# Optimization experiments

Measured on AMD Instinct MI355X. Metric: run time of the kernel, lower is better.

The kernel has to match this reference:

```python
import jax, jax.numpy as jnp
import numpy as np

NEG_BIG = -9e15
ALPHA = 0.2  # leakyrelu negative slope

N, F_IN, F_OUT = 8192, 512, 64


def setup_inputs() -> dict:
    key = jax.random.key(0)
    k1, k2, k3, k4 = jax.random.split(key, 4)
    input = jax.random.normal(k1, (N, F_IN), dtype=jnp.float32)
    adj = jax.random.randint(k2, (N, N), 0, 2, dtype=jnp.int32)
    W = jax.random.normal(k3, (F_IN, F_OUT), dtype=jnp.float32) * 0.05
    a = jax.random.normal(k4, (2 * F_OUT, 1), dtype=jnp.float32) * 0.1
    return {"input": input, "adj": adj, "W": W, "a": a}


def reference(input, adj, W, a):
    # h: [N, F_out]
    h = input @ W
    # The original builds a_input[i,j] = concat(h_i, h_j) and dots with a.
    # Decompose: e_ij = leakyrelu(h_i @ a_src + h_j @ a_dst) -- identical math,
    # avoids the N*N*2F intermediate.
    a_src = a[:F_OUT, 0]  # [F_out]
    a_dst = a[F_OUT:, 0]  # [F_out]
    s_src = h @ a_src     # [N]
    s_dst = h @ a_dst     # [N]
    e = jax.nn.leaky_relu(s_src[:, None] + s_dst[None, :], negative_slope=ALPHA)  # [N, N]
    masked = jnp.where(adj > 0, e, jnp.float32(NEG_BIG))
    attention = jax.nn.softmax(masked, axis=1)  # dropout omitted (eval mode)
    h_prime = attention @ h  # [N, F_out]
    return jax.nn.elu(h_prime)  # concat=True
```

## Files before the change

kernel.cpp:

```cpp
#include <hip/hip_runtime.h>
#include <hip/hip_bf16.h>

namespace {
constexpr int kN    = 8192;
constexpr int kFin  = 512;
constexpr int kFout = 64;
constexpr float kAlpha = 0.2f;
constexpr int kJSplit = 4;
constexpr int kJLen   = kN / kJSplit;
constexpr int kChunks = kJLen / 128;

using bf16x8 = __attribute__((ext_vector_type(8))) short;
using f32x4  = __attribute__((ext_vector_type(4))) float;

__device__ __forceinline__ unsigned short f2bf(float x) {
  return __builtin_bit_cast(unsigned short, __float2bfloat16(x));
}
__device__ __forceinline__ float lrelu(float x) {
  return fmaxf(x, kAlpha * x);
}
__device__ __forceinline__ unsigned int fkey(float x) {
  unsigned int b = __float_as_uint(x);
  return (b & 0x80000000u) ? ~b : (b | 0x80000000u);
}
__device__ __forceinline__ float fdec(unsigned int k) {
  return (k & 0x80000000u) ? __uint_as_float(k ^ 0x80000000u) : __uint_as_float(~k);
}
}

__global__ __launch_bounds__(256) void k_wt(const float* __restrict__ W,
                                            float* __restrict__ WT,
                                            unsigned int* __restrict__ Smax_u) {
  const int gid = blockIdx.x * 256 + threadIdx.x;
  if (gid == 0) *Smax_u = 0u;
  const int k = gid >> 6, f = gid & 63;
  WT[(size_t)f * kFin + k] = W[gid];
}

__global__ __launch_bounds__(256) void k_linear(
    const float* __restrict__ X, const float* __restrict__ WT, const float* __restrict__ A,
    unsigned short* __restrict__ hTf, float* __restrict__ s_src, float* __restrict__ s_dst,
    unsigned int* __restrict__ Smax_u)
{
  const int t = threadIdx.x;
  const int wv = t >> 6, f = t & 63;
  const int i0 = blockIdx.x * 16;

  __shared__ float Xlds[16 * kFin];
  __shared__ unsigned short h_sm[16][64];
  __shared__ float red[4];

  {
    const float4* Xg = (const float4*)(X + (size_t)i0 * kFin);
    float4* Xl = (float4*)Xlds;
    float4 v0 = Xg[t +   0], v1 = Xg[t + 256], v2 = Xg[t +  512], v3 = Xg[t +  768];
    float4 v4 = Xg[t +1024], v5 = Xg[t +1280], v6 = Xg[t + 1536], v7 = Xg[t + 1792];
    Xl[t +    0] = v0; Xl[t +  256] = v1; Xl[t +  512] = v2; Xl[t +  768] = v3;
    Xl[t + 1024] = v4; Xl[t + 1280] = v5; Xl[t + 1536] = v6; Xl[t + 1792] = v7;
  }
  __syncthreads();

  const int r0l = wv * 4;
  const float* w0 = WT + (size_t)f * kFin;
  float acc0 = 0.f, acc1 = 0.f, acc2 = 0.f, acc3 = 0.f;
  float4 wb0 = *(const float4*)(w0 + 0);
  float4 wb1 = *(const float4*)(w0 + 4);
  const float* xr = Xlds + r0l * kFin;
  for (int k = 0; k < kFin; k += 4) {
    const float4 wc = (k & 4) ? wb1 : wb0;
    if (k + 8 < kFin) {
      const float4 wn = *(const float4*)(w0 + k + 8);
      if (k & 4) wb1 = wn; else wb0 = wn;
    }
    const float4 xa = *(const float4*)(xr + k);
    const float4 xb = *(const float4*)(xr + kFin + k);
    const float4 xc = *(const float4*)(xr + 2 * kFin + k);
    const float4 xd = *(const float4*)(xr + 3 * kFin + k);
#pragma unroll
    for (int j = 0; j < 4; ++j) {
      const float wk = ((const float*)&wc)[j];
      acc0 = fmaf(((const float*)&xa)[j], wk, acc0);
      acc1 = fmaf(((const float*)&xb)[j], wk, acc1);
      acc2 = fmaf(((const float*)&xc)[j], wk, acc2);
      acc3 = fmaf(((const float*)&xd)[j], wk, acc3);
    }
  }

  const float asrc = A[f], adst = A[kFout + f];
  float accs[4] = {acc0, acc1, acc2, acc3};
  float dmax = -3.4e38f;
#pragma unroll
  for (int r = 0; r < 4; ++r) {
    float vs = accs[r] * asrc;
    float vd = accs[r] * adst;
#pragma unroll
    for (int off = 32; off > 0; off >>= 1) {
      vs += __shfl_xor(vs, off, 64);
      vd += __shfl_xor(vd, off, 64);
    }
    if (f == 0) {
      s_src[i0 + r0l + r] = vs;
      s_dst[i0 + r0l + r] = vd;
      dmax = fmaxf(dmax, vd);
    }
    h_sm[r0l + r][f] = f2bf(accs[r]);
  }
  if (f == 0) red[wv] = dmax;
  __syncthreads();
  if (t == 0) {
    float m = fmaxf(fmaxf(red[0], red[1]), fmaxf(red[2], red[3]));
    atomicMax(Smax_u, fkey(m));
  }

  if (t < 128) {
    const int jblk = i0 >> 5, half = (i0 >> 4) & 1;
    const int w = t >> 5, li = t & 31;
    const int lane = half * 32 + li;
    const int ql = li >> 4, fcol = w * 16 + (li & 15);
    bf16x8 v;
#pragma unroll
    for (int e = 0; e < 8; ++e) v[e] = (short)h_sm[ql * 8 + e][fcol];
    *(bf16x8*)(hTf + (size_t)jblk * 2048 + w * 512 + (size_t)lane * 8) = v;
  }
}

__global__ __launch_bounds__(256) void k_attn(
    const int* __restrict__ adj, const unsigned short* __restrict__ hTf,
    const float* __restrict__ s_src, const float* __restrict__ s_dst,
    const unsigned int* __restrict__ Smax_u, float* __restrict__ accp,
    float* __restrict__ lp)
{
  const int t = threadIdx.x;
  const int wv = t >> 6, lane = t & 63;
  const int b = blockIdx.x;
  const int i0 = (b >> 2) * 16;
  const int jbase = (b & 3) * kJLen;
  const int pr = t >> 4, jb = t & 15;

  __shared__ unsigned short Plds[2][16][136];

  const float S = fdec(*Smax_u);
  const float ssrc = s_src[i0 + pr];
  const float mr = lrelu(ssrc + S);

  float l_acc = 0.f;
  f32x4 acc = {0.f, 0.f, 0.f, 0.f};

  const int4*   aptr = (const int4*)(adj + (size_t)(i0 + pr) * kN + jbase + jb * 8);
  const float4* dptr = (const float4*)(s_dst + jbase + jb * 8);
  const unsigned short* hbase = hTf + (size_t)(jbase >> 5) * 2048 + wv * 512 + (size_t)lane * 8;

  const int mrow = lane & 15, quad = lane >> 4;

  int4   A0a = aptr[0],  A1a = aptr[1];
  float4 D0a = dptr[0],  D1a = dptr[1];
  int4   A0b = aptr[32], A1b = aptr[33];
  float4 D0b = dptr[32], D1b = dptr[33];

  auto phase = [&](int c, int sbuf, int4& A0, int4& A1, float4& D0, float4& D1)
      __attribute__((always_inline)) {
    float pv[8];
    {
      const int* aa = (const int*)&A0;
      const float* dd = (const float*)&D0;
#pragma unroll
      for (int j = 0; j < 4; ++j) {
        const float e = lrelu(ssrc + dd[j]);
        pv[j] = aa[j] > 0 ? __expf(e - mr) : 0.f;
      }
      aa = (const int*)&A1; dd = (const float*)&D1;
#pragma unroll
      for (int j = 0; j < 4; ++j) {
        const float e = lrelu(ssrc + dd[j]);
        pv[4 + j] = aa[j] > 0 ? __expf(e - mr) : 0.f;
      }
    }
    bf16x8 ps;
#pragma unroll
    for (int j = 0; j < 8; ++j) {
      l_acc += pv[j];
      ps[j] = (short)f2bf(pv[j]);
    }
    *(bf16x8*)&Plds[sbuf][pr][jb * 8] = ps;

    const uint4 hv0 = *(const uint4*)(hbase + (size_t)(c * 4 + 0) * 2048);
    const uint4 hv1 = *(const uint4*)(hbase + (size_t)(c * 4 + 1) * 2048);
    const uint4 hv2 = *(const uint4*)(hbase + (size_t)(c * 4 + 2) * 2048);
    const uint4 hv3 = *(const uint4*)(hbase + (size_t)(c * 4 + 3) * 2048);

    if (c + 2 < kChunks) {
      A0 = aptr[(c + 2) * 32]; A1 = aptr[(c + 2) * 32 + 1];
      D0 = dptr[(c + 2) * 32]; D1 = dptr[(c + 2) * 32 + 1];
    }
    __syncthreads();

    acc = __builtin_amdgcn_mfma_f32_16x16x32_bf16(
        *(const bf16x8*)&Plds[sbuf][mrow][0 * 32 + quad * 8], __builtin_bit_cast(bf16x8, hv0), acc, 0, 0, 0);
    acc = __builtin_amdgcn_mfma_f32_16x16x32_bf16(
        *(const bf16x8*)&Plds[sbuf][mrow][1 * 32 + quad * 8], __builtin_bit_cast(bf16x8, hv1), acc, 0, 0, 0);
    acc = __builtin_amdgcn_mfma_f32_16x16x32_bf16(
        *(const bf16x8*)&Plds[sbuf][mrow][2 * 32 + quad * 8], __builtin_bit_cast(bf16x8, hv2), acc, 0, 0, 0);
    acc = __builtin_amdgcn_mfma_f32_16x16x32_bf16(
        *(const bf16x8*)&Plds[sbuf][mrow][3 * 32 + quad * 8], __builtin_bit_cast(bf16x8, hv3), acc, 0, 0, 0);
  };

  for (int c = 0; c < kChunks; c += 2) {
    phase(c,     0, A0a, A1a, D0a, D1a);
    phase(c + 1, 1, A0b, A1b, D0b, D1b);
  }

  float lv = l_acc;
  lv += __shfl_xor(lv, 8, 64);
  lv += __shfl_xor(lv, 4, 64);
  lv += __shfl_xor(lv, 2, 64);
  lv += __shfl_xor(lv, 1, 64);
  if (jb == 0) lp[(size_t)b * 16 + pr] = lv;

  float* ab = accp + (size_t)b * 16 * 64;
#pragma unroll
  for (int reg = 0; reg < 4; ++reg) {
    ab[(quad * 4 + reg) * 64 + wv * 16 + mrow] = acc[reg];
  }
}

__global__ __launch_bounds__(256) void k_comb(const float* __restrict__ accp,
                                              const float* __restrict__ lp,
                                              float* __restrict__ out)
{
  const int gid = blockIdx.x * 256 + threadIdx.x;
  const int i = gid >> 6, f = gid & 63;
  const int ib = i >> 4, il = i & 15;
  const int b0 = ib * kJSplit;
  float a = 0.f, l = 0.f;
#pragma unroll
  for (int q = 0; q < kJSplit; ++q) {
    a += accp[((size_t)(b0 + q) * 16 + il) * 64 + f];
    l += lp[(size_t)(b0 + q) * 16 + il];
  }
  float v = a / l;
  v = v > 0.f ? v : __expf(v) - 1.f;
  out[gid] = v;
}

extern "C" void kernel_launch(void* const* d_in, const int* in_sizes, int n_in,
                              void* d_out, int out_size, void* d_ws, size_t ws_size,
                              hipStream_t stream) {
  const float* X   = (const float*)d_in[0];
  const int*   adj = (const int*)d_in[1];
  const float* W   = (const float*)d_in[2];
  const float* A   = (const float*)d_in[3];
  float* out = (float*)d_out;

  char* ws = (char*)d_ws;
  unsigned short* hTf = (unsigned short*)ws;  ws += (size_t)kN * kFout * 2;
  float* WT    = (float*)ws;                  ws += (size_t)kFout * kFin * 4;
  float* s_src = (float*)ws;                  ws += kN * 4;
  float* s_dst = (float*)ws;                  ws += kN * 4;
  unsigned int* Smax_u = (unsigned int*)ws;   ws += 256;
  float* accp  = (float*)ws;                  ws += (size_t)(kN / 16) * kJSplit * 16 * 64 * 4;
  float* lp    = (float*)ws;

  k_wt    <<<kFin * kFout / 256, 256, 0, stream>>>(W, WT, Smax_u);
  k_linear<<<kN / 16, 256, 0, stream>>>(X, WT, A, hTf, s_src, s_dst, Smax_u);
  k_attn  <<<(kN / 16) * kJSplit, 256, 0, stream>>>(adj, hTf, s_src, s_dst, Smax_u, accp, lp);
  k_comb  <<<kN * kFout / 256, 256, 0, stream>>>(accp, lp, out);
}
```

Baseline: 411.7 us.

## Make each wave compute its own P fragment in registers, dropping the LDS exchange

```diff
diff --git a/kernel.cpp b/kernel.cpp
--- a/kernel.cpp
+++ b/kernel.cpp
@@ -6,9 +6,10 @@
 constexpr int kFin  = 512;
 constexpr int kFout = 64;
 constexpr float kAlpha = 0.2f;
-constexpr int kJSplit = 4;
+constexpr int kJSplit = 8;
 constexpr int kJLen   = kN / kJSplit;
-constexpr int kChunks = kJLen / 128;
+constexpr int kChunks = kJLen / 32;
+constexpr int kTileParts = 2;
 
 using bf16x8 = __attribute__((ext_vector_type(8))) short;
 using f32x4  = __attribute__((ext_vector_type(4))) float;
@@ -132,36 +133,45 @@
 {
   const int t = threadIdx.x;
   const int wv = t >> 6, lane = t & 63;
-  const int b = blockIdx.x;
-  const int i0 = (b >> 2) * 16;
-  const int jbase = (b & 3) * kJLen;
-  const int pr = t >> 4, jb = t & 15;
-
-  __shared__ unsigned short Plds[2][16][136];
+  const int wid = blockIdx.x * 4 + wv;
+  const int tile = wid >> 3;
+  const int q    = wid & 7;
+  const int i0 = tile * 16, jbase = q * kJLen;
+  const int row = lane & 15, quad = lane >> 4;
+
+  __shared__ float sacc[4][16][64];
+  __shared__ float sl[4][16];
 
   const float S = fdec(*Smax_u);
-  const float ssrc = s_src[i0 + pr];
+  const float ssrc = s_src[i0 + row];
   const float mr = lrelu(ssrc + S);
 
+  const int4*   aptr = (const int4*)(adj + (size_t)(i0 + row) * kN + jbase + quad * 8);
+  const float4* dptr = (const float4*)(s_dst + jbase + quad * 8);
+  const unsigned short* hbase = hTf + (size_t)(jbase >> 5) * 2048 + (size_t)lane * 8;
+
   float l_acc = 0.f;
-  f32x4 acc = {0.f, 0.f, 0.f, 0.f};
-
-  const int4*   aptr = (const int4*)(adj + (size_t)(i0 + pr) * kN + jbase + jb * 8);
-  const float4* dptr = (const float4*)(s_dst + jbase + jb * 8);
-  const unsigned short* hbase = hTf + (size_t)(jbase >> 5) * 2048 + wv * 512 + (size_t)lane * 8;
-
-  const int mrow = lane & 15, quad = lane >> 4;
-
-  int4   A0a = aptr[0],  A1a = aptr[1];
-  float4 D0a = dptr[0],  D1a = dptr[1];
-  int4   A0b = aptr[32], A1b = aptr[33];
-  float4 D0b = dptr[32], D1b = dptr[33];
-
-  auto phase = [&](int c, int sbuf, int4& A0, int4& A1, float4& D0, float4& D1)
+  f32x4 acc0 = {0.f, 0.f, 0.f, 0.f};
+  f32x4 acc1 = {0.f, 0.f, 0.f, 0.f};
+  f32x4 acc2 = {0.f, 0.f, 0.f, 0.f};
+  f32x4 acc3 = {0.f, 0.f, 0.f, 0.f};
+
+  int4   Aa0 = aptr[0],  Aa1 = aptr[1];
+  float4 Da0 = dptr[0],  Da1 = dptr[1];
+  int4   Ab0 = aptr[8],  Ab1 = aptr[9];
+  float4 Db0 = dptr[8],  Db1 = dptr[9];
+
+  auto body = [&](int c, int4& A0, int4& A1, float4& D0, float4& D1)
       __attribute__((always_inline)) {
+    const unsigned short* hp = hbase + (size_t)c * 2048;
+    const uint4 hv0 = *(const uint4*)(hp +    0);
+    const uint4 hv1 = *(const uint4*)(hp +  512);
+    const uint4 hv2 = *(const uint4*)(hp + 1024);
+    const uint4 hv3 = *(const uint4*)(hp + 1536);
+
     float pv[8];
     {
-      const int* aa = (const int*)&A0;
+      const int*   aa = (const int*)&A0;
       const float* dd = (const float*)&D0;
 #pragma unroll
       for (int j = 0; j < 4; ++j) {
@@ -175,51 +185,59 @@
         pv[4 + j] = aa[j] > 0 ? __expf(e - mr) : 0.f;
       }
     }
-    bf16x8 ps;
-#pragma unroll
-    for (int j = 0; j < 8; ++j) {
-      l_acc += pv[j];
-      ps[j] = (short)f2bf(pv[j]);
-    }
-    *(bf16x8*)&Plds[sbuf][pr][jb * 8] = ps;
-
-    const uint4 hv0 = *(const uint4*)(hbase + (size_t)(c * 4 + 0) * 2048);
-    const uint4 hv1 = *(const uint4*)(hbase + (size_t)(c * 4 + 1) * 2048);
-    const uint4 hv2 = *(const uint4*)(hbase + (size_t)(c * 4 + 2) * 2048);
-    const uint4 hv3 = *(const uint4*)(hbase + (size_t)(c * 4 + 3) * 2048);
-
-    if (c + 2 < kChunks) {
-      A0 = aptr[(c + 2) * 32]; A1 = aptr[(c + 2) * 32 + 1];
-      D0 = dptr[(c + 2) * 32]; D1 = dptr[(c + 2) * 32 + 1];
-    }
-    __syncthreads();
-
-    acc = __builtin_amdgcn_mfma_f32_16x16x32_bf16(
-        *(const bf16x8*)&Plds[sbuf][mrow][0 * 32 + quad * 8], __builtin_bit_cast(bf16x8, hv0), acc, 0, 0, 0);
-    acc = __builtin_amdgcn_mfma_f32_16x16x32_bf16(
-        *(const bf16x8*)&Plds[sbuf][mrow][1 * 32 + quad * 8], __builtin_bit_cast(bf16x8, hv1), acc, 0, 0, 0);
-    acc = __builtin_amdgcn_mfma_f32_16x16x32_bf16(
-        *(const bf16x8*)&Plds[sbuf][mrow][2 * 32 + quad * 8], __builtin_bit_cast(bf16x8, hv2), acc, 0, 0, 0);
-    acc = __builtin_amdgcn_mfma_f32_16x16x32_bf16(
-        *(const bf16x8*)&Plds[sbuf][mrow][3 * 32 + quad * 8], __builtin_bit_cast(bf16x8, hv3), acc, 0, 0, 0);
+
+    {
+      const int cn = (c + 2) & (kChunks - 1);
+      A0 = aptr[cn * 8];  A1 = aptr[cn * 8 + 1];
+      D0 = dptr[cn * 8];  D1 = dptr[cn * 8 + 1];
+    }
+
+    l_acc += ((pv[0] + pv[1]) + (pv[2] + pv[3])) +
+             ((pv[4] + pv[5]) + (pv[6] + pv[7]));
+    bf16x8 pa;
+#pragma unroll
+    for (int j = 0; j < 8; ++j) pa[j] = (short)f2bf(pv[j]);
+
+    acc0 = __builtin_amdgcn_mfma_f32_16x16x32_bf16(pa, __builtin_bit_cast(bf16x8, hv0), acc0, 0, 0, 0);
+    acc1 = __builtin_amdgcn_mfma_f32_16x16x32_bf16(pa, __builtin_bit_cast(bf16x8, hv1), acc1, 0, 0, 0);
+    acc2 = __builtin_amdgcn_mfma_f32_16x16x32_bf16(pa, __builtin_bit_cast(bf16x8, hv2), acc2, 0, 0, 0);
+    acc3 = __builtin_amdgcn_mfma_f32_16x16x32_bf16(pa, __builtin_bit_cast(bf16x8, hv3), acc3, 0, 0, 0);
   };
 
   for (int c = 0; c < kChunks; c += 2) {
-    phase(c,     0, A0a, A1a, D0a, D1a);
-    phase(c + 1, 1, A0b, A1b, D0b, D1b);
+    body(c,     Aa0, Aa1, Da0, Da1);
+    body(c + 1, Ab0, Ab1, Db0, Db1);
   }
 
   float lv = l_acc;
-  lv += __shfl_xor(lv, 8, 64);
-  lv += __shfl_xor(lv, 4, 64);
-  lv += __shfl_xor(lv, 2, 64);
-  lv += __shfl_xor(lv, 1, 64);
-  if (jb == 0) lp[(size_t)b * 16 + pr] = lv;
-
-  float* ab = accp + (size_t)b * 16 * 64;
-#pragma unroll
-  for (int reg = 0; reg < 4; ++reg) {
-    ab[(quad * 4 + reg) * 64 + wv * 16 + mrow] = acc[reg];
+  lv += __shfl_xor(lv, 16, 64);
+  lv += __shfl_xor(lv, 32, 64);
+  if (lane < 16) sl[wv][lane] = lv;
+
+  {
+    float* ab = &sacc[wv][0][0];
+#pragma unroll
+    for (int reg = 0; reg < 4; ++reg) {
+      ab[(quad * 4 + reg) * 64 +  0 + row] = acc0[reg];
+      ab[(quad * 4 + reg) * 64 + 16 + row] = acc1[reg];
+      ab[(quad * 4 + reg) * 64 + 32 + row] = acc2[reg];
+      ab[(quad * 4 + reg) * 64 + 48 + row] = acc3[reg];
+    }
+  }
+  __syncthreads();
+
+  {
+    const float* sb = &sacc[0][0][0];
+    float* gout = accp + (size_t)blockIdx.x * 16 * 64;
+#pragma unroll
+    for (int k = 0; k < 4; ++k) {
+      const int idx = t + k * 256;
+      gout[idx] = (sb[idx] + sb[1024 + idx]) + (sb[2048 + idx] + sb[3072 + idx]);
+    }
+    if (t < 16) {
+      lp[(size_t)blockIdx.x * 16 + t] =
+          (sl[0][t] + sl[1][t]) + (sl[2][t] + sl[3][t]);
+    }
   }
 }
 
@@ -230,12 +248,12 @@
   const int gid = blockIdx.x * 256 + threadIdx.x;
   const int i = gid >> 6, f = gid & 63;
   const int ib = i >> 4, il = i & 15;
-  const int b0 = ib * kJSplit;
+  const int b0 = ib * kTileParts;
   float a = 0.f, l = 0.f;
 #pragma unroll
-  for (int q = 0; q < kJSplit; ++q) {
-    a += accp[((size_t)(b0 + q) * 16 + il) * 64 + f];
-    l += lp[(size_t)(b0 + q) * 16 + il];
+  for (int p = 0; p < kTileParts; ++p) {
+    a += accp[((size_t)(b0 + p) * 16 + il) * 64 + f];
+    l += lp[(size_t)(b0 + p) * 16 + il];
   }
   float v = a / l;
   v = v > 0.f ? v : __expf(v) - 1.f;
@@ -257,11 +275,11 @@
   float* s_src = (float*)ws;                  ws += kN * 4;
   float* s_dst = (float*)ws;                  ws += kN * 4;
   unsigned int* Smax_u = (unsigned int*)ws;   ws += 256;
-  float* accp  = (float*)ws;                  ws += (size_t)(kN / 16) * kJSplit * 16 * 64 * 4;
+  float* accp  = (float*)ws;                  ws += (size_t)(kN / 16) * kTileParts * 16 * 64 * 4;
   float* lp    = (float*)ws;
 
   k_wt    <<<kFin * kFout / 256, 256, 0, stream>>>(W, WT, Smax_u);
   k_linear<<<kN / 16, 256, 0, stream>>>(X, WT, A, hTf, s_src, s_dst, Smax_u);
-  k_attn  <<<(kN / 16) * kJSplit, 256, 0, stream>>>(adj, hTf, s_src, s_dst, Smax_u, accp, lp);
+  k_attn  <<<(kN / 16) * kJSplit / 4, 256, 0, stream>>>(adj, hTf, s_src, s_dst, Smax_u, accp, lp);
   k_comb  <<<kN * kFout / 256, 256, 0, stream>>>(accp, lp, out);
 }
```

New measurement: 443.2 us. 7.7% more time.
